# Performance work log

Measured on AMD Instinct MI355X. Metric: run time of the kernel, lower is better.

## Reference

```python
import jax, jax.numpy as jnp
import numpy as np

S, R, DH = 8, 2, 64  # num_searches, num_retrievals, dim_head


def setup_inputs() -> dict:
    key = jax.random.key(0)
    ks = jax.random.split(key, 7)
    b, n, dim = 2, 2048, 512
    def w(k, i, o):
        return jax.random.normal(k, (i, o), dtype=jnp.float32) / np.sqrt(i)
    return {
        "x": jax.random.normal(ks[0], (b, n, dim), dtype=jnp.float32),
        "wq_s": w(ks[1], dim, S * DH),
        "wk_s": w(ks[2], dim, S * DH),
        "wv_r": w(ks[3], dim, R * DH),
        "wq_r": w(ks[4], dim, S * DH),
        "wk_ret": w(ks[5], DH, DH),
        "w_out": w(ks[6], S * DH, dim),
    }


def reference(x, wq_s, wk_s, wv_r, wq_r, wk_ret, w_out):
    b, n, dim = x.shape
    scale = DH ** -0.5
    # stage 1: search attention over sequence, per search head s
    sq = (x @ wq_s).reshape(b, n, S, DH).transpose(0, 2, 1, 3) * scale  # b s n d
    sk = (x @ wk_s).reshape(b, n, S, DH).transpose(0, 2, 1, 3)          # b s n d
    rv = (x @ wv_r).reshape(b, n, R, DH).transpose(0, 2, 1, 3)          # b r n d
    search_sim = jnp.einsum('bsid,bsjd->bsij', sq, sk)                  # b s n n
    search_attn = jax.nn.softmax(search_sim, axis=-1)
    # retrieved values: each search head attends into each retrieval's values
    retrieved = jnp.einsum('bsij,brjd->bsird', search_attn, rv)         # b s n r d
    # stage 2: retrieval composition (softmax over the r retrievals)
    rq = (x @ wq_r).reshape(b, n, S, DH).transpose(0, 2, 1, 3) * scale  # b s n d
    rk = retrieved @ wk_ret                                             # b s n r d
    retrieval_sim = jnp.einsum('bsid,bsird->bsir', rq, rk)              # b s n r
    retrieval_attn = jax.nn.softmax(retrieval_sim, axis=-1)
    out = jnp.einsum('bsir,bsird->bsid', retrieval_attn, retrieved)     # b s n d
    out = out.transpose(0, 2, 1, 3).reshape(b, n, S * DH)               # b n (s d)
    return out @ w_out
```

## Files before the change

### kernel.cpp

```cpp
#include <hip/hip_runtime.h>
#include <hip/hip_bf16.h>

#define DEV __device__ __forceinline__

typedef __attribute__((ext_vector_type(8))) short bf16x8;
typedef __attribute__((ext_vector_type(4))) float f32x4;

DEV float b2f(unsigned short u) {
    unsigned int v = ((unsigned int)u) << 16;
    float f; __builtin_memcpy(&f, &v, 4); return f;
}
DEV unsigned short f2b(float f) {
    unsigned int v; __builtin_memcpy(&v, &f, 4);
    v = (v + 0x7fffu + ((v >> 16) & 1u)) >> 16;
    return (unsigned short)v;
}
DEV unsigned short f2b_hw(float f) {
    __hip_bfloat16 h = __float2bfloat16(f);
    unsigned short u; __builtin_memcpy(&u, &h, 2); return u;
}
DEV float exp2raw(float x) { return __builtin_amdgcn_exp2f(x); }

DEV f32x4 mfma16(bf16x8 a, bf16x8 b, f32x4 c) {
    return __builtin_amdgcn_mfma_f32_16x16x32_bf16(a, b, c, 0, 0, 0);
}

DEV void stage16(const void* g, void* l) {
    __builtin_amdgcn_global_load_lds((const __attribute__((address_space(1))) void*)g,
                                     (__attribute__((address_space(3))) void*)l, 16, 0, 0);
}

#define WAIT_VM6()  asm volatile("s_waitcnt vmcnt(6)" ::: "memory")
#define WAIT_VM3()  asm volatile("s_waitcnt vmcnt(3)" ::: "memory")
#define WAIT_VM0()  asm volatile("s_waitcnt vmcnt(0)" ::: "memory")
#define WAIT_LGKM() asm volatile("s_waitcnt lgkmcnt(0)" ::: "memory")
#define BAR()       __builtin_amdgcn_s_barrier()
#define SCHED()     __builtin_amdgcn_sched_barrier(0)

constexpr float SCALE_L2E = 0.125f * 1.44269504088896340736f;

__global__ void k_elem(const float* __restrict__ x,
                       const float* __restrict__ wk_ret,
                       unsigned short* __restrict__ xb,
                       unsigned short* __restrict__ wkt)
{
    const int T1 = 4096 * 512;
    const int T4 = 64 * 64;
    const int total = T1 + T4;
    for (int idx = blockIdx.x * blockDim.x + threadIdx.x; idx < total;
         idx += gridDim.x * blockDim.x) {
        if (idx < T1) xb[idx] = f2b(x[idx]);
        else          wkt[idx - T1] = f2b(wk_ret[idx - T1]);
    }
}

__global__ __launch_bounds__(256) void k_trans(const float* __restrict__ wq_s,
                                               const float* __restrict__ wk_s,
                                               const float* __restrict__ wv_r,
                                               const float* __restrict__ wq_r,
                                               const float* __restrict__ w_out,
                                               unsigned short* __restrict__ wt,
                                               unsigned short* __restrict__ wot)
{
    __shared__ float tl[32][33];
    int m = blockIdx.x;
    const float* src; unsigned short* dst;
    int base, srcld, kt, nt;
    if (m < 256)      { src = wq_s;  dst = wt;  base = 0;    srcld = 512; kt = m >> 4; nt = m & 15; }
    else if (m < 512) { m -= 256; src = wk_s;  dst = wt;  base = 512;  srcld = 512; kt = m >> 4; nt = m & 15; }
    else if (m < 576) { m -= 512; src = wv_r;  dst = wt;  base = 1024; srcld = 128; kt = m >> 2; nt = m & 3; }
    else if (m < 832) { m -= 576; src = wq_r;  dst = wt;  base = 1152; srcld = 512; kt = m >> 4; nt = m & 15; }
    else              { m -= 832; src = w_out; dst = wot; base = 0;    srcld = 512; kt = m >> 4; nt = m & 15; }

    const int r = threadIdx.x >> 5, c = threadIdx.x & 31;
#pragma unroll
    for (int s = 0; s < 4; ++s) {
        int rr = r + 8 * s;
        tl[rr][c] = src[(size_t)(kt * 32 + rr) * srcld + nt * 32 + c];
    }
    __syncthreads();
#pragma unroll
    for (int s = 0; s < 4; ++s) {
        int rr = r + 8 * s;
        dst[(size_t)(base + nt * 32 + rr) * 512 + kt * 32 + c] = f2b(tl[c][rr]);
    }
}

template<int EPI>
__global__ __launch_bounds__(256, 2) void k_gemm(const unsigned short* __restrict__ A,
                                                 const unsigned short* __restrict__ Bt,
                                                 unsigned short* __restrict__ qs,
                                                 unsigned short* __restrict__ ks,
                                                 unsigned short* __restrict__ rqb,
                                                 unsigned short* __restrict__ vt,
                                                 float* __restrict__ out)
{
    __shared__ unsigned char ab_lds[49152];

    const int tid = threadIdx.x;
    const int lane = tid & 63, wid = tid >> 6;
    const int lr = lane & 15, lg = lane >> 4;
    const int wr = wid >> 1, wc = wid & 1;
    const int brow0 = blockIdx.x * 128;
    const int bcol0 = blockIdx.y * 64;

    const int sub = lane >> 3;
    const int chk = lane & 7;
    const int scs = chk ^ sub;

    const f32x4 z = {0.f, 0.f, 0.f, 0.f};
    f32x4 acc[4][2];
#pragma unroll
    for (int m = 0; m < 4; ++m)
#pragma unroll
        for (int n = 0; n < 2; ++n) acc[m][n] = z;

    const unsigned short* Ab = A + (size_t)brow0 * 512;

    auto STAGE = [&](int buf, int k0) {
        unsigned char* ab = ab_lds + buf * 16384;
        unsigned char* bb = ab_lds + 32768 + buf * 8192;
#pragma unroll
        for (int ii = 0; ii < 4; ++ii) {
            int r0 = wid * 32 + ii * 8;
            const unsigned short* g = Ab + (size_t)(r0 + sub) * 512 + k0 + scs * 8;
            stage16(g, ab + r0 * 128);
        }
#pragma unroll
        for (int ii = 0; ii < 2; ++ii) {
            int r0 = wid * 16 + ii * 8;
            const unsigned short* g = Bt + (size_t)(bcol0 + r0 + sub) * 512 + k0 + scs * 8;
            stage16(g, bb + r0 * 128);
        }
    };

    auto COMPUTE = [&](const int cur) {
        const unsigned char* ab = ab_lds + cur * 16384;
        const unsigned char* bb = ab_lds + 32768 + cur * 8192;
#pragma unroll
        for (int ksb = 0; ksb < 2; ++ksb) {
            const int c = ksb * 4 + lg;
            bf16x8 bfr[2];
#pragma unroll
            for (int n = 0; n < 2; ++n) {
                int row = wc * 32 + n * 16 + lr;
                bfr[n] = *(const bf16x8*)(bb + row * 128 + ((c ^ (row & 7)) << 4));
            }
#pragma unroll
            for (int m = 0; m < 4; ++m) {
                int row = wr * 64 + m * 16 + lr;
                bf16x8 af = *(const bf16x8*)(ab + row * 128 + ((c ^ (row & 7)) << 4));
                acc[m][0] = mfma16(af, bfr[0], acc[m][0]);
                acc[m][1] = mfma16(af, bfr[1], acc[m][1]);
            }
        }
    };

    STAGE(0, 0);
#pragma unroll 1
    for (int it = 0; it < 3; ++it) {
        STAGE(1, (2 * it + 1) * 64);
        WAIT_VM6(); BAR(); SCHED();
        COMPUTE(0);
        WAIT_LGKM(); SCHED(); BAR(); SCHED();
        STAGE(0, (2 * it + 2) * 64);
        WAIT_VM6(); BAR(); SCHED();
        COMPUTE(1);
        WAIT_LGKM(); SCHED(); BAR(); SCHED();
    }
    STAGE(1, 7 * 64);
    WAIT_VM6(); BAR(); SCHED();
    COMPUTE(0);
    WAIT_LGKM(); SCHED(); BAR(); SCHED();
    WAIT_VM0(); BAR(); SCHED();
    COMPUTE(1);

#pragma unroll
    for (int m = 0; m < 4; ++m) {
#pragma unroll
        for (int n = 0; n < 2; ++n) {
#pragma unroll
            for (int i = 0; i < 4; ++i) {
                int gr = brow0 + wr * 64 + m * 16 + lg * 4 + i;
                int gc = bcol0 + wc * 32 + n * 16 + lr;
                float v = acc[m][n][i];
                if (EPI == 1) {
                    out[(size_t)gr * 512 + gc] = v;
                } else {
                    int b = gr >> 11, in = gr & 2047;
                    if (gc < 512) {
                        int s = gc >> 6, d = gc & 63;
                        qs[((b * 8 + s) * 2048 + in) * 64 + d] = f2b(v * SCALE_L2E);
                    } else if (gc < 1024) {
                        int cgc = gc - 512; int s = cgc >> 6, d = cgc & 63;
                        ks[((b * 8 + s) * 2048 + in) * 64 + d] = f2b(v);
                    } else if (gc < 1152) {
                        int cgc = gc - 1024;
                        vt[(b * 128 + cgc) * 2048 + in] = f2b(v);
                    } else {
                        int cgc = gc - 1152; int s = cgc >> 6, d = cgc & 63;
                        rqb[((b * 8 + s) * 2048 + in) * 64 + d] = f2b(v * SCALE_L2E);
                    }
                }
            }
        }
    }
}

__global__ __launch_bounds__(512, 4) void k_attn(const unsigned short* __restrict__ qs,
                                                 const unsigned short* __restrict__ ks,
                                                 const unsigned short* __restrict__ rqb,
                                                 const unsigned short* __restrict__ vt,
                                                 const unsigned short* __restrict__ wkt,
                                                 unsigned short* __restrict__ ob)
{
    __shared__ unsigned char kv_lds[49152];

    const int tid = threadIdx.x;
    const int lane = tid & 63, wid = tid >> 6;
    const int lr = lane & 15, lg = lane >> 4;
    const int qsub = wid & 3, h = wid >> 2;
    const int bid = blockIdx.x;
    const int bs = bid >> 5, qt = bid & 31;
    const int gb = bs >> 3, gs = bs & 7;
    const int qrow0 = qt * 64 + qsub * 16;

    const int sub = lane >> 3;
    const int scs = (lane & 7) ^ sub;

    const unsigned short* qbase = qs + ((size_t)bs * 2048 + qrow0 + lr) * 64 + lg * 8;
    const bf16x8 q0 = *(const bf16x8*)(qbase);
    const bf16x8 q1 = *(const bf16x8*)(qbase + 32);

    const unsigned short* kbase = ks + (size_t)bs * 131072;
    const unsigned short* vbase = vt + (size_t)gb * 262144;

    const f32x4 z = {0.f, 0.f, 0.f, 0.f};

    float m_r = -3.0e38f;
    float acc_l = 0.f;
    f32x4 acc[8];
#pragma unroll
    for (int c8 = 0; c8 < 8; ++c8) acc[c8] = z;

    const int rk0 = h * 32 + (lr >> 2) * 8 + (lr & 3);
    const int rk1 = rk0 + 4;
    const int ko0a = rk0 * 128 + ((lg ^ (rk0 & 7)) << 4);
    const int ko0b = rk0 * 128 + (((lg + 4) ^ (rk0 & 7)) << 4);
    const int ko1a = rk1 * 128 + ((lg ^ (rk1 & 7)) << 4);
    const int ko1b = rk1 * 128 + (((lg + 4) ^ (rk1 & 7)) << 4);
    const int vx = (((h * 4 + lg) ^ (lr & 7)) << 4) + lr * 128;

    const unsigned short* sp[3];
    int step[3], loff[3];
#pragma unroll
    for (int j = 0; j < 3; ++j) {
        int s = wid * 3 + j;
        if (s < 8) { sp[j] = kbase + (size_t)(s * 8 + sub) * 64 + scs * 8;          step[j] = 4096; }
        else       { sp[j] = vbase + (size_t)((s - 8) * 8 + sub) * 2048 + scs * 8;  step[j] = 64;   }
        loff[j] = s * 1024;
    }

    auto STAGE = [&](const int buf) {
        unsigned char* base = kv_lds + buf * 24576;
#pragma unroll
        for (int j = 0; j < 3; ++j) {
            stage16(sp[j], base + loff[j]);
            sp[j] += step[j];
        }
    };

    auto COMPUTE = [&](const int cur) {
        const unsigned char* kb = kv_lds + cur * 24576;
        const unsigned char* vb = kb + 8192;

        f32x4 s[2];
        __builtin_amdgcn_s_setprio(1);
        {
            bf16x8 kf0 = *(const bf16x8*)(kb + ko0a);
            bf16x8 kf1 = *(const bf16x8*)(kb + ko0b);
            f32x4 t = z;
            t = mfma16(kf0, q0, t);
            t = mfma16(kf1, q1, t);
            s[0] = t;
        }
        {
            bf16x8 kf0 = *(const bf16x8*)(kb + ko1a);
            bf16x8 kf1 = *(const bf16x8*)(kb + ko1b);
            f32x4 t = z;
            t = mfma16(kf0, q0, t);
            t = mfma16(kf1, q1, t);
            s[1] = t;
        }
        __builtin_amdgcn_s_setprio(0);

        float lm = fmaxf(fmaxf(fmaxf(s[0][0], s[0][1]), fmaxf(s[0][2], s[0][3])),
                         fmaxf(fmaxf(s[1][0], s[1][1]), fmaxf(s[1][2], s[1][3])));
        if (__any(lm > m_r + 8.0f)) {
            float mx = fmaxf(lm, __shfl_xor(lm, 16));
            mx = fmaxf(mx, __shfl_xor(mx, 32));
            float m_new = fmaxf(m_r, mx);
            float alpha = exp2raw(m_r - m_new);
            float al[4];
#pragma unroll
            for (int i = 0; i < 4; ++i) al[i] = __shfl(alpha, lg * 4 + i, 16);
#pragma unroll
            for (int c8 = 0; c8 < 8; ++c8)
#pragma unroll
                for (int i = 0; i < 4; ++i) acc[c8][i] *= al[i];
            acc_l *= alpha;
            m_r = m_new;
        }

        float p[8];
#pragma unroll
        for (int a = 0; a < 2; ++a)
#pragma unroll
            for (int i = 0; i < 4; ++i)
                p[a * 4 + i] = exp2raw(s[a][i] - m_r);
        acc_l += ((p[0] + p[1]) + (p[2] + p[3])) + ((p[4] + p[5]) + (p[6] + p[7]));
        unsigned int pu[4];
#pragma unroll
        for (int t2 = 0; t2 < 4; ++t2)
            asm("v_cvt_pk_bf16_f32 %0, %1, %2" : "=v"(pu[t2]) : "v"(p[2 * t2]), "v"(p[2 * t2 + 1]));
        bf16x8 pa;
        __builtin_memcpy(&pa, pu, 16);

        __builtin_amdgcn_s_setprio(1);
#pragma unroll
        for (int c8 = 0; c8 < 8; ++c8) {
            bf16x8 vf = *(const bf16x8*)(vb + c8 * 2048 + vx);
            acc[c8] = mfma16(pa, vf, acc[c8]);
        }
        __builtin_amdgcn_s_setprio(0);
    };

    STAGE(0);

#pragma unroll 1
    for (int it = 0; it < 15; ++it) {
        STAGE(1);
        WAIT_VM3(); BAR(); SCHED();
        COMPUTE(0);
        WAIT_LGKM(); SCHED(); BAR(); SCHED();
        STAGE(0);
        WAIT_VM3(); BAR(); SCHED();
        COMPUTE(1);
        WAIT_LGKM(); SCHED(); BAR(); SCHED();
    }
    STAGE(1);
    WAIT_VM3(); BAR(); SCHED();
    COMPUTE(0);
    WAIT_LGKM(); SCHED(); BAR(); SCHED();
    WAIT_VM0(); BAR(); SCHED();
    COMPUTE(1);

    float l2 = acc_l + __shfl_xor(acc_l, 16);
    float l_row = l2 + __shfl_xor(l2, 32);

    __syncthreads();
    float* mrg = (float*)kv_lds;
    float* ml  = (float*)(kv_lds + 33792);
    if (h == 1) {
#pragma unroll
        for (int c8 = 0; c8 < 8; ++c8)
#pragma unroll
            for (int i = 0; i < 4; ++i)
                mrg[(qsub * 16 + lg * 4 + i) * 132 + c8 * 16 + lr] = acc[c8][i];
        if (lane < 16) {
            ml[(qsub * 16 + lane) * 2 + 0] = m_r;
            ml[(qsub * 16 + lane) * 2 + 1] = l_row;
        }
    }
    __syncthreads();
    if (h == 1) return;

    float m_own[4], l_own[4];
#pragma unroll
    for (int i = 0; i < 4; ++i) {
        m_own[i] = __shfl(m_r,  lg * 4 + i, 16);
        l_own[i] = __shfl(l_row, lg * 4 + i, 16);
    }

    float inv[4];
    f32x4 accM[8];
#pragma unroll
    for (int i = 0; i < 4; ++i) {
        float m_b = ml[(qsub * 16 + lg * 4 + i) * 2 + 0];
        float l_b = ml[(qsub * 16 + lg * 4 + i) * 2 + 1];
        float m_new = fmaxf(m_own[i], m_b);
        float fa = exp2raw(m_own[i] - m_new);
        float fb = exp2raw(m_b - m_new);
        inv[i] = 1.0f / (l_own[i] * fa + l_b * fb);
#pragma unroll
        for (int c8 = 0; c8 < 8; ++c8)
            accM[c8][i] = acc[c8][i] * fa + mrg[(qsub * 16 + lg * 4 + i) * 132 + c8 * 16 + lr] * fb;
    }

    const unsigned short* rqbase = rqb + ((size_t)bs * 2048 + qrow0 + lr) * 64 + lg * 8;
    const bf16x8 rq0 = *(const bf16x8*)(rqbase);
    const bf16x8 rq1 = *(const bf16x8*)(rqbase + 32);

    f32x4 Tt[4];
#pragma unroll
    for (int ct = 0; ct < 4; ++ct) {
        bf16x8 wb0 = *(const bf16x8*)(wkt + (ct * 16 + lr) * 64 + lg * 8);
        bf16x8 wb1 = *(const bf16x8*)(wkt + (ct * 16 + lr) * 64 + 32 + lg * 8);
        f32x4 t = z;
        t = mfma16(rq0, wb0, t);
        t = mfma16(rq1, wb1, t);
        Tt[ct] = t;
    }

    float w0v[4], w1v[4];
#pragma unroll
    for (int i = 0; i < 4; ++i) {
        float s0 = 0.f, s1 = 0.f;
#pragma unroll
        for (int ct = 0; ct < 4; ++ct) {
            s0 += Tt[ct][i] * accM[ct][i];
            s1 += Tt[ct][i] * accM[4 + ct][i];
        }
        s0 *= inv[i]; s1 *= inv[i];
        s0 += __shfl_xor(s0, 1, 16); s1 += __shfl_xor(s1, 1, 16);
        s0 += __shfl_xor(s0, 2, 16); s1 += __shfl_xor(s1, 2, 16);
        s0 += __shfl_xor(s0, 4, 16); s1 += __shfl_xor(s1, 4, 16);
        s0 += __shfl_xor(s0, 8, 16); s1 += __shfl_xor(s1, 8, 16);
        float mm = fmaxf(s0, s1);
        float e0 = exp2raw(s0 - mm), e1 = exp2raw(s1 - mm);
        float inw = 1.0f / (e0 + e1);
        w0v[i] = e0 * inw; w1v[i] = e1 * inw;
    }

#pragma unroll
    for (int ct = 0; ct < 4; ++ct) {
#pragma unroll
        for (int i = 0; i < 4; ++i) {
            float o = (w0v[i] * accM[ct][i] + w1v[i] * accM[4 + ct][i]) * inv[i];
            ob[((size_t)gb * 2048 + qrow0 + lg * 4 + i) * 512 + gs * 64 + ct * 16 + lr] = f2b_hw(o);
        }
    }
}

extern "C" void kernel_launch(void* const* d_in, const int* in_sizes, int n_in,
                              void* d_out, int out_size, void* d_ws, size_t ws_size,
                              hipStream_t stream)
{
    (void)in_sizes; (void)n_in; (void)out_size; (void)ws_size;
    const float* x      = (const float*)d_in[0];
    const float* wq_s   = (const float*)d_in[1];
    const float* wk_s   = (const float*)d_in[2];
    const float* wv_r   = (const float*)d_in[3];
    const float* wq_r   = (const float*)d_in[4];
    const float* wk_ret = (const float*)d_in[5];
    const float* w_out  = (const float*)d_in[6];

    char* ws = (char*)d_ws;
    unsigned short* xb  = (unsigned short*)(ws + 0);
    unsigned short* wt  = (unsigned short*)(ws + 4194304);
    unsigned short* qsb = (unsigned short*)(ws + 5898240);
    unsigned short* ksb = (unsigned short*)(ws + 10092544);
    unsigned short* rqb = (unsigned short*)(ws + 14286848);
    unsigned short* vtb = (unsigned short*)(ws + 18481152);
    unsigned short* obb = (unsigned short*)(ws + 19529728);
    unsigned short* wot = (unsigned short*)(ws + 23724032);
    unsigned short* wkt = (unsigned short*)(ws + 24248320);

    hipLaunchKernelGGL(k_elem, dim3(1024), dim3(256), 0, stream,
                       x, wk_ret, xb, wkt);
    hipLaunchKernelGGL(k_trans, dim3(1088), dim3(256), 0, stream,
                       wq_s, wk_s, wv_r, wq_r, w_out, wt, wot);
    hipLaunchKernelGGL((k_gemm<0>), dim3(32, 26), dim3(256), 0, stream,
                       xb, wt, qsb, ksb, rqb, vtb, (float*)nullptr);
    hipLaunchKernelGGL(k_attn, dim3(512), dim3(512), 0, stream,
                       qsb, ksb, rqb, vtb, wkt, obb);
    hipLaunchKernelGGL((k_gemm<1>), dim3(32, 8), dim3(256), 0, stream,
                       obb, wot, (unsigned short*)nullptr, (unsigned short*)nullptr,
                       (unsigned short*)nullptr, (unsigned short*)nullptr, (float*)d_out);
}
```

Measured before the change: 76.62 us.

## Halve attention block to 4 waves, each processing two 16-row query tiles

The attention kernel now launches 256 threads per block instead of 512, and each wave handles 32 query rows as two 16-row MFMA tiles. Each K fragment read from LDS is reused across both tiles, and each V fragment across both accumulators, which halves LDS reads per unit of MMA work. Each thread now stages six K/V chunks instead of three, with the wait count raised to match, and the LDS swizzle is changed to suit the new access pattern. In exchange, register use per wave roughly doubles (two accumulator sets) and there are fewer waves per block to hide latency, so occupancy may drop.

```diff
diff --git a/kernel.cpp b/kernel.cpp
--- a/kernel.cpp
+++ b/kernel.cpp
@@ -31,7 +31,6 @@
 }
 
 #define WAIT_VM6()  asm volatile("s_waitcnt vmcnt(6)" ::: "memory")
-#define WAIT_VM3()  asm volatile("s_waitcnt vmcnt(3)" ::: "memory")
 #define WAIT_VM0()  asm volatile("s_waitcnt vmcnt(0)" ::: "memory")
 #define WAIT_LGKM() asm volatile("s_waitcnt lgkmcnt(0)" ::: "memory")
 #define BAR()       __builtin_amdgcn_s_barrier()
@@ -207,7 +206,7 @@
     }
 }
 
-__global__ __launch_bounds__(512, 4) void k_attn(const unsigned short* __restrict__ qs,
+__global__ __launch_bounds__(256, 3) void k_attn(const unsigned short* __restrict__ qs,
                                                  const unsigned short* __restrict__ ks,
                                                  const unsigned short* __restrict__ rqb,
                                                  const unsigned short* __restrict__ vt,
@@ -219,43 +218,52 @@
     const int tid = threadIdx.x;
     const int lane = tid & 63, wid = tid >> 6;
     const int lr = lane & 15, lg = lane >> 4;
-    const int qsub = wid & 3, h = wid >> 2;
+    const int qsub = wid & 1, h = wid >> 1;
     const int bid = blockIdx.x;
     const int bs = bid >> 5, qt = bid & 31;
     const int gb = bs >> 3, gs = bs & 7;
-    const int qrow0 = qt * 64 + qsub * 16;
+    const int qrow0 = qt * 64 + qsub * 32;
 
     const int sub = lane >> 3;
-    const int scs = (lane & 7) ^ sub;
-
-    const unsigned short* qbase = qs + ((size_t)bs * 2048 + qrow0 + lr) * 64 + lg * 8;
-    const bf16x8 q0 = *(const bf16x8*)(qbase);
-    const bf16x8 q1 = *(const bf16x8*)(qbase + 32);
+
+    bf16x8 q0[2], q1[2];
+#pragma unroll
+    for (int j = 0; j < 2; ++j) {
+        const unsigned short* qb = qs + ((size_t)bs * 2048 + qrow0 + j * 16 + lr) * 64 + lg * 8;
+        q0[j] = *(const bf16x8*)(qb);
+        q1[j] = *(const bf16x8*)(qb + 32);
+    }
 
     const unsigned short* kbase = ks + (size_t)bs * 131072;
     const unsigned short* vbase = vt + (size_t)gb * 262144;
 
     const f32x4 z = {0.f, 0.f, 0.f, 0.f};
 
-    float m_r = -3.0e38f;
-    float acc_l = 0.f;
-    f32x4 acc[8];
-#pragma unroll
-    for (int c8 = 0; c8 < 8; ++c8) acc[c8] = z;
-
+    float m_r[2] = {-3.0e38f, -3.0e38f};
+    float acc_l[2] = {0.f, 0.f};
+    f32x4 acc[2][8];
+#pragma unroll
+    for (int j = 0; j < 2; ++j)
+#pragma unroll
+        for (int c8 = 0; c8 < 8; ++c8) acc[j][c8] = z;
+
+    const int fb  = ((lr >> 2) & 1) << 2;
+    const int f0  = (lr & 3) ^ fb;
+    const int f1  = ((lr & 3) | 4) ^ fb;
     const int rk0 = h * 32 + (lr >> 2) * 8 + (lr & 3);
     const int rk1 = rk0 + 4;
-    const int ko0a = rk0 * 128 + ((lg ^ (rk0 & 7)) << 4);
-    const int ko0b = rk0 * 128 + (((lg + 4) ^ (rk0 & 7)) << 4);
-    const int ko1a = rk1 * 128 + ((lg ^ (rk1 & 7)) << 4);
-    const int ko1b = rk1 * 128 + (((lg + 4) ^ (rk1 & 7)) << 4);
-    const int vx = (((h * 4 + lg) ^ (lr & 7)) << 4) + lr * 128;
-
-    const unsigned short* sp[3];
-    int step[3], loff[3];
-#pragma unroll
-    for (int j = 0; j < 3; ++j) {
-        int s = wid * 3 + j;
+    const int ko0a = rk0 * 128 + ((lg ^ f0) << 4);
+    const int ko0b = rk0 * 128 + (((lg + 4) ^ f0) << 4);
+    const int ko1a = rk1 * 128 + ((lg ^ f1) << 4);
+    const int ko1b = rk1 * 128 + (((lg + 4) ^ f1) << 4);
+    const int vx = lr * 128 + (((h * 4 + lg) ^ (lr & 7) ^ ((lr >> 3) << 2)) << 4);
+
+    const unsigned short* sp[6];
+    int step[6], loff[6];
+#pragma unroll
+    for (int j = 0; j < 6; ++j) {
+        int s = wid * 6 + j;
+        int scs = (lane & 7) ^ sub ^ ((s & 1) << 2);
         if (s < 8) { sp[j] = kbase + (size_t)(s * 8 + sub) * 64 + scs * 8;          step[j] = 4096; }
         else       { sp[j] = vbase + (size_t)((s - 8) * 8 + sub) * 2048 + scs * 8;  step[j] = 64;   }
         loff[j] = s * 1024;
@@ -264,7 +272,7 @@
     auto STAGE = [&](const int buf) {
         unsigned char* base = kv_lds + buf * 24576;
 #pragma unroll
-        for (int j = 0; j < 3; ++j) {
+        for (int j = 0; j < 6; ++j) {
             stage16(sp[j], base + loff[j]);
             sp[j] += step[j];
         }
@@ -274,63 +282,74 @@
         const unsigned char* kb = kv_lds + cur * 24576;
         const unsigned char* vb = kb + 8192;
 
-        f32x4 s[2];
+        f32x4 s[2][2];
         __builtin_amdgcn_s_setprio(1);
         {
-            bf16x8 kf0 = *(const bf16x8*)(kb + ko0a);
-            bf16x8 kf1 = *(const bf16x8*)(kb + ko0b);
-            f32x4 t = z;
-            t = mfma16(kf0, q0, t);
-            t = mfma16(kf1, q1, t);
-            s[0] = t;
-        }
-        {
-            bf16x8 kf0 = *(const bf16x8*)(kb + ko1a);
-            bf16x8 kf1 = *(const bf16x8*)(kb + ko1b);
-            f32x4 t = z;
-            t = mfma16(kf0, q0, t);
-            t = mfma16(kf1, q1, t);
-            s[1] = t;
+            bf16x8 k0a = *(const bf16x8*)(kb + ko0a);
+            bf16x8 k0b = *(const bf16x8*)(kb + ko0b);
+            bf16x8 k1a = *(const bf16x8*)(kb + ko1a);
+            bf16x8 k1b = *(const bf16x8*)(kb + ko1b);
+#pragma unroll
+            for (int j = 0; j < 2; ++j) {
+                f32x4 t = z;
+                t = mfma16(k0a, q0[j], t);
+                t = mfma16(k0b, q1[j], t);
+                s[j][0] = t;
+                t = z;
+                t = mfma16(k1a, q0[j], t);
+                t = mfma16(k1b, q1[j], t);
+                s[j][1] = t;
+            }
         }
         __builtin_amdgcn_s_setprio(0);
 
-        float lm = fmaxf(fmaxf(fmaxf(s[0][0], s[0][1]), fmaxf(s[0][2], s[0][3])),
-                         fmaxf(fmaxf(s[1][0], s[1][1]), fmaxf(s[1][2], s[1][3])));
-        if (__any(lm > m_r + 8.0f)) {
-            float mx = fmaxf(lm, __shfl_xor(lm, 16));
-            mx = fmaxf(mx, __shfl_xor(mx, 32));
-            float m_new = fmaxf(m_r, mx);
-            float alpha = exp2raw(m_r - m_new);
-            float al[4];
-#pragma unroll
-            for (int i = 0; i < 4; ++i) al[i] = __shfl(alpha, lg * 4 + i, 16);
-#pragma unroll
-            for (int c8 = 0; c8 < 8; ++c8)
-#pragma unroll
-                for (int i = 0; i < 4; ++i) acc[c8][i] *= al[i];
-            acc_l *= alpha;
-            m_r = m_new;
-        }
-
-        float p[8];
-#pragma unroll
-        for (int a = 0; a < 2; ++a)
-#pragma unroll
-            for (int i = 0; i < 4; ++i)
-                p[a * 4 + i] = exp2raw(s[a][i] - m_r);
-        acc_l += ((p[0] + p[1]) + (p[2] + p[3])) + ((p[4] + p[5]) + (p[6] + p[7]));
-        unsigned int pu[4];
-#pragma unroll
-        for (int t2 = 0; t2 < 4; ++t2)
-            asm("v_cvt_pk_bf16_f32 %0, %1, %2" : "=v"(pu[t2]) : "v"(p[2 * t2]), "v"(p[2 * t2 + 1]));
-        bf16x8 pa;
-        __builtin_memcpy(&pa, pu, 16);
+        float lm[2];
+#pragma unroll
+        for (int j = 0; j < 2; ++j)
+            lm[j] = fmaxf(fmaxf(fmaxf(s[j][0][0], s[j][0][1]), fmaxf(s[j][0][2], s[j][0][3])),
+                          fmaxf(fmaxf(s[j][1][0], s[j][1][1]), fmaxf(s[j][1][2], s[j][1][3])));
+        if (__any((lm[0] > m_r[0] + 8.0f) || (lm[1] > m_r[1] + 8.0f))) {
+#pragma unroll
+            for (int j = 0; j < 2; ++j) {
+                float mx = fmaxf(lm[j], __shfl_xor(lm[j], 16));
+                mx = fmaxf(mx, __shfl_xor(mx, 32));
+                float m_new = fmaxf(m_r[j], mx);
+                float alpha = exp2raw(m_r[j] - m_new);
+                float al[4];
+#pragma unroll
+                for (int i = 0; i < 4; ++i) al[i] = __shfl(alpha, lg * 4 + i, 16);
+#pragma unroll
+                for (int c8 = 0; c8 < 8; ++c8)
+#pragma unroll
+                    for (int i = 0; i < 4; ++i) acc[j][c8][i] *= al[i];
+                acc_l[j] *= alpha;
+                m_r[j] = m_new;
+            }
+        }
+
+        bf16x8 pa[2];
+#pragma unroll
+        for (int j = 0; j < 2; ++j) {
+            float p[8];
+#pragma unroll
+            for (int a = 0; a < 2; ++a)
+#pragma unroll
+                for (int i = 0; i < 4; ++i)
+                    p[a * 4 + i] = exp2raw(s[j][a][i] - m_r[j]);
+            acc_l[j] += ((p[0] + p[1]) + (p[2] + p[3])) + ((p[4] + p[5]) + (p[6] + p[7]));
+            unsigned int pu[4];
+#pragma unroll
+            for (int t2 = 0; t2 < 4; ++t2)
+                asm("v_cvt_pk_bf16_f32 %0, %1, %2" : "=v"(pu[t2]) : "v"(p[2 * t2]), "v"(p[2 * t2 + 1]));
+            __builtin_memcpy(&pa[j], pu, 16);
+        }
 
         __builtin_amdgcn_s_setprio(1);
 #pragma unroll
         for (int c8 = 0; c8 < 8; ++c8) {
             bf16x8 vf = *(const bf16x8*)(vb + c8 * 2048 + vx);
-            acc[c8] = mfma16(pa, vf, acc[c8]);
+            acc[0][c8] = mfma16(pa[0], vf, acc[0][c8]);
+            acc[1][c8] = mfma16(pa[1], vf, acc[1][c8]);
         }
         __builtin_amdgcn_s_setprio(0);
     };
@@ -340,104 +359,115 @@
 #pragma unroll 1
     for (int it = 0; it < 15; ++it) {
         STAGE(1);
-        WAIT_VM3(); BAR(); SCHED();
+        WAIT_VM6(); BAR(); SCHED();
         COMPUTE(0);
         WAIT_LGKM(); SCHED(); BAR(); SCHED();
         STAGE(0);
-        WAIT_VM3(); BAR(); SCHED();
+        WAIT_VM6(); BAR(); SCHED();
         COMPUTE(1);
         WAIT_LGKM(); SCHED(); BAR(); SCHED();
     }
     STAGE(1);
-    WAIT_VM3(); BAR(); SCHED();
+    WAIT_VM6(); BAR(); SCHED();
     COMPUTE(0);
     WAIT_LGKM(); SCHED(); BAR(); SCHED();
     WAIT_VM0(); BAR(); SCHED();
     COMPUTE(1);
 
-    float l2 = acc_l + __shfl_xor(acc_l, 16);
-    float l_row = l2 + __shfl_xor(l2, 32);
+    float l_row[2];
+#pragma unroll
+    for (int j = 0; j < 2; ++j) {
+        float l2 = acc_l[j] + __shfl_xor(acc_l[j], 16);
+        l_row[j] = l2 + __shfl_xor(l2, 32);
+    }
 
     __syncthreads();
     float* mrg = (float*)kv_lds;
     float* ml  = (float*)(kv_lds + 33792);
     if (h == 1) {
 #pragma unroll
-        for (int c8 = 0; c8 < 8; ++c8)
-#pragma unroll
-            for (int i = 0; i < 4; ++i)
-                mrg[(qsub * 16 + lg * 4 + i) * 132 + c8 * 16 + lr] = acc[c8][i];
-        if (lane < 16) {
-            ml[(qsub * 16 + lane) * 2 + 0] = m_r;
-            ml[(qsub * 16 + lane) * 2 + 1] = l_row;
+        for (int j = 0; j < 2; ++j) {
+#pragma unroll
+            for (int c8 = 0; c8 < 8; ++c8)
+#pragma unroll
+                for (int i = 0; i < 4; ++i)
+                    mrg[(qsub * 32 + j * 16 + lg * 4 + i) * 132 + c8 * 16 + lr] = acc[j][c8][i];
+            if (lane < 16) {
+                ml[(qsub * 32 + j * 16 + lane) * 2 + 0] = m_r[j];
+                ml[(qsub * 32 + j * 16 + lane) * 2 + 1] = l_row[j];
+            }
         }
     }
     __syncthreads();
     if (h == 1) return;
 
-    float m_own[4], l_own[4];
-#pragma unroll
-    for (int i = 0; i < 4; ++i) {
-        m_own[i] = __shfl(m_r,  lg * 4 + i, 16);
-        l_own[i] = __shfl(l_row, lg * 4 + i, 16);
-    }
-
-    float inv[4];
-    f32x4 accM[8];
-#pragma unroll
-    for (int i = 0; i < 4; ++i) {
-        float m_b = ml[(qsub * 16 + lg * 4 + i) * 2 + 0];
-        float l_b = ml[(qsub * 16 + lg * 4 + i) * 2 + 1];
-        float m_new = fmaxf(m_own[i], m_b);
-        float fa = exp2raw(m_own[i] - m_new);
-        float fb = exp2raw(m_b - m_new);
-        inv[i] = 1.0f / (l_own[i] * fa + l_b * fb);
-#pragma unroll
-        for (int c8 = 0; c8 < 8; ++c8)
-            accM[c8][i] = acc[c8][i] * fa + mrg[(qsub * 16 + lg * 4 + i) * 132 + c8 * 16 + lr] * fb;
-    }
-
-    const unsigned short* rqbase = rqb + ((size_t)bs * 2048 + qrow0 + lr) * 64 + lg * 8;
-    const bf16x8 rq0 = *(const bf16x8*)(rqbase);
-    const bf16x8 rq1 = *(const bf16x8*)(rqbase + 32);
-
-    f32x4 Tt[4];
-#pragma unroll
-    for (int ct = 0; ct < 4; ++ct) {
-        bf16x8 wb0 = *(const bf16x8*)(wkt + (ct * 16 + lr) * 64 + lg * 8);
-        bf16x8 wb1 = *(const bf16x8*)(wkt + (ct * 16 + lr) * 64 + 32 + lg * 8);
-        f32x4 t = z;
-        t = mfma16(rq0, wb0, t);
-        t = mfma16(rq1, wb1, t);
-        Tt[ct] = t;
-    }
-
-    float w0v[4], w1v[4];
-#pragma unroll
-    for (int i = 0; i < 4; ++i) {
-        float s0 = 0.f, s1 = 0.f;
+#pragma unroll
+    for (int j = 0; j < 2; ++j) {
+        float m_own[4], l_own[4];
+#pragma unroll
+        for (int i = 0; i < 4; ++i) {
+            m_own[i] = __shfl(m_r[j],  lg * 4 + i, 16);
+            l_own[i] = __shfl(l_row[j], lg * 4 + i, 16);
+        }
+
+        float inv[4];
+        f32x4 accM[8];
+#pragma unroll
+        for (int i = 0; i < 4; ++i) {
+            int row = qsub * 32 + j * 16 + lg * 4 + i;
+            float m_b = ml[row * 2 + 0];
+            float l_b = ml[row * 2 + 1];
+            float m_new = fmaxf(m_own[i], m_b);
+            float fa = exp2raw(m_own[i] - m_new);
+            float fb2 = exp2raw(m_b - m_new);
+            inv[i] = 1.0f / (l_own[i] * fa + l_b * fb2);
+#pragma unroll
+            for (int c8 = 0; c8 < 8; ++c8)
+                accM[c8][i] = acc[j][c8][i] * fa + mrg[row * 132 + c8 * 16 + lr] * fb2;
+        }
+
+        const unsigned short* rqbase = rqb + ((size_t)bs * 2048 + qrow0 + j * 16 + lr) * 64 + lg * 8;
+        const bf16x8 rq0 = *(const bf16x8*)(rqbase);
+        const bf16x8 rq1 = *(const bf16x8*)(rqbase + 32);
+
+        f32x4 Tt[4];
 #pragma unroll
         for (int ct = 0; ct < 4; ++ct) {
-            s0 += Tt[ct][i] * accM[ct][i];
-            s1 += Tt[ct][i] * accM[4 + ct][i];
-        }
-        s0 *= inv[i]; s1 *= inv[i];
-        s0 += __shfl_xor(s0, 1, 16); s1 += __shfl_xor(s1, 1, 16);
-        s0 += __shfl_xor(s0, 2, 16); s1 += __shfl_xor(s1, 2, 16);
-        s0 += __shfl_xor(s0, 4, 16); s1 += __shfl_xor(s1, 4, 16);
-        s0 += __shfl_xor(s0, 8, 16); s1 += __shfl_xor(s1, 8, 16);
-        float mm = fmaxf(s0, s1);
-        float e0 = exp2raw(s0 - mm), e1 = exp2raw(s1 - mm);
-        float inw = 1.0f / (e0 + e1);
-        w0v[i] = e0 * inw; w1v[i] = e1 * inw;
-    }
-
-#pragma unroll
-    for (int ct = 0; ct < 4; ++ct) {
+            bf16x8 wb0 = *(const bf16x8*)(wkt + (ct * 16 + lr) * 64 + lg * 8);
+            bf16x8 wb1 = *(const bf16x8*)(wkt + (ct * 16 + lr) * 64 + 32 + lg * 8);
+            f32x4 t = z;
+            t = mfma16(rq0, wb0, t);
+            t = mfma16(rq1, wb1, t);
+            Tt[ct] = t;
+        }
+
+        float w0v[4], w1v[4];
 #pragma unroll
         for (int i = 0; i < 4; ++i) {
-            float o = (w0v[i] * accM[ct][i] + w1v[i] * accM[4 + ct][i]) * inv[i];
-            ob[((size_t)gb * 2048 + qrow0 + lg * 4 + i) * 512 + gs * 64 + ct * 16 + lr] = f2b_hw(o);
+            float s0 = 0.f, s1 = 0.f;
+#pragma unroll
+            for (int ct = 0; ct < 4; ++ct) {
+                s0 += Tt[ct][i] * accM[ct][i];
+                s1 += Tt[ct][i] * accM[4 + ct][i];
+            }
+            s0 *= inv[i]; s1 *= inv[i];
+            s0 += __shfl_xor(s0, 1, 16); s1 += __shfl_xor(s1, 1, 16);
+            s0 += __shfl_xor(s0, 2, 16); s1 += __shfl_xor(s1, 2, 16);
+            s0 += __shfl_xor(s0, 4, 16); s1 += __shfl_xor(s1, 4, 16);
+            s0 += __shfl_xor(s0, 8, 16); s1 += __shfl_xor(s1, 8, 16);
+            float mm = fmaxf(s0, s1);
+            float e0 = exp2raw(s0 - mm), e1 = exp2raw(s1 - mm);
+            float inw = 1.0f / (e0 + e1);
+            w0v[i] = e0 * inw; w1v[i] = e1 * inw;
+        }
+
+#pragma unroll
+        for (int ct = 0; ct < 4; ++ct) {
+#pragma unroll
+            for (int i = 0; i < 4; ++i) {
+                float o = (w0v[i] * accM[ct][i] + w1v[i] * accM[4 + ct][i]) * inv[i];
+                ob[((size_t)gb * 2048 + qrow0 + j * 16 + lg * 4 + i) * 512 + gs * 64 + ct * 16 + lr] = f2b_hw(o);
+            }
         }
     }
 }
@@ -472,7 +502,7 @@
                        wq_s, wk_s, wv_r, wq_r, w_out, wt, wot);
     hipLaunchKernelGGL((k_gemm<0>), dim3(32, 26), dim3(256), 0, stream,
                        xb, wt, qsb, ksb, rqb, vtb, (float*)nullptr);
-    hipLaunchKernelGGL(k_attn, dim3(512), dim3(512), 0, stream,
+    hipLaunchKernelGGL(k_attn, dim3(512), dim3(256), 0, stream,
                        qsb, ksb, rqb, vtb, wkt, obb);
     hipLaunchKernelGGL((k_gemm<1>), dim3(32, 8), dim3(256), 0, stream,
                        obb, wot, (unsigned short*)nullptr, (unsigned short*)nullptr,
```

New measurement: 121.5 us. 58.6% more time.
